# Kernel tuning notes

Measured on AMD Instinct MI355X. Metric: run time of the kernel, lower is better.

## Reference

```python
import jax, jax.numpy as jnp
import numpy as np

N_NODES = 110
C = 4096  # in_channels = hidden = out_channels


def setup_inputs() -> dict:
    key = jax.random.key(0)
    ks = jax.random.split(key, 8)
    x = jax.random.normal(ks[0], (N_NODES, C), dtype=jnp.float32)
    adj = jax.random.randint(ks[1], (N_NODES, N_NODES), 0, 2, dtype=jnp.int32)
    # torch.nn.Linear weights stored [out_features, in_features]
    W2 = jax.random.normal(ks[2], (C, C), dtype=jnp.float32) / np.sqrt(C)
    b2 = jax.random.normal(ks[3], (C,), dtype=jnp.float32) * 0.01
    W1 = jax.random.normal(ks[4], (2 * C, C), dtype=jnp.float32) / np.sqrt(2 * C)
    b1 = jax.random.normal(ks[5], (C,), dtype=jnp.float32) * 0.01
    Wl = jax.random.normal(ks[6], (N_NODES, N_NODES), dtype=jnp.float32) / np.sqrt(N_NODES)
    bl = jax.random.normal(ks[7], (N_NODES,), dtype=jnp.float32) * 0.01
    # note: W1 is stored [in=2C, out=C]; W2 [in=C, out=C]; Wl [in=110, out=110]
    return {"x": x, "adj": adj, "W2": W2, "b2": b2, "W1": W1, "b1": b1, "Wl": Wl, "bl": bl}


def reference(x, adj, W2, b2, W1, b1, Wl, bl):
    # FeatGraphConv: h = lin2(x)
    h = x @ W2 + b2  # [N, C]
    # edge_index.nonzero(): adjacency -> edge list (i=src, j=dst); mean-aggregate
    # h[src] at dst. Dense equivalent: column-normalized mask matmul.
    mask = (adj != 0).astype(x.dtype)  # [N, N]
    deg = mask.sum(axis=0)  # in-degree of each target node j
    aggr = (mask.T @ h) / jnp.maximum(deg, 1.0)[:, None]  # [N, C]; 0 for isolated nodes (PyG mean)
    # update: lin1(cat(h, aggr)) then relu (in RegGNN.forward)
    out = jax.nn.relu(jnp.concatenate([h, aggr], axis=1) @ W1 + b1)  # [N, C]
    # x.t(); lin(110,110); x.t()
    out = (out.T @ Wl.T + bl).T  # [N, C]
    return out
```

## Files before the change

### kernel.cpp

```cpp
#include <hip/hip_runtime.h>
#include <hip/hip_fp16.h>

#define C 4096
#define NN 110
#define MPAD 112
#define BN 128
#define BK 64
#define KCHUNK 512
#define NIT (KCHUNK / BK)
#define LDSTR 72
#define BSTR 64

typedef _Float16 f16x8 __attribute__((ext_vector_type(8)));
typedef float fx4 __attribute__((ext_vector_type(4)));

__global__ __launch_bounds__(256)
void prep1_kernel(const float* __restrict__ x, _Float16* __restrict__ A1) {
    int idx = blockIdx.x * 256 + threadIdx.x;
    int n = idx >> 11;
    union { _Float16 h[2]; unsigned u; } pk;
    pk.u = 0;
    if (n < NN) {
        float2 v = *(const float2*)(x + 2 * (size_t)idx);
        pk.h[0] = (_Float16)v.x;
        pk.h[1] = (_Float16)v.y;
    }
    ((unsigned*)A1)[idx] = pk.u;
}

__global__ __launch_bounds__(256, 2)
void mm_kernel(const _Float16* __restrict__ A, const float* __restrict__ B,
               float* __restrict__ Cacc, int lda) {
    __shared__ _Float16 As[2][MPAD * LDSTR];
    __shared__ _Float16 Bs[2][BN * BSTR];

    const int t    = threadIdx.x;
    const int j0   = blockIdx.x * BN;
    const int k0   = blockIdx.y * KCHUNK;
    const int w    = t >> 6;
    const int L    = t & 63;
    const int l15  = L & 15;
    const int q    = L >> 4;
    const int bc   = t & 127;
    const int bgq  = t >> 7;
    const int bswz = bc & 7;

    int arow[4], ako[4];
    bool aval[4];
#pragma unroll
    for (int i = 0; i < 4; ++i) {
        int idx = t + i * 256;
        aval[i] = (idx < MPAD * (BK / 8));
        int id2 = aval[i] ? idx : 0;
        arow[i] = id2 >> 3;
        ako[i]  = (id2 & 7) << 3;
    }

    fx4 acc[7][2];
#pragma unroll
    for (int mt = 0; mt < 7; ++mt)
#pragma unroll
        for (int nt = 0; nt < 2; ++nt)
            acc[mt][nt] = (fx4){0.f, 0.f, 0.f, 0.f};

    f16x8 av[4];
    float bv[32];

#define STAGE(kc_)                                                             \
    {                                                                          \
        _Pragma("unroll")                                                      \
        for (int i = 0; i < 4; ++i)                                            \
            av[i] = *(const f16x8*)(A + (size_t)arow[i] * lda + (k0 + (kc_)) + ako[i]); \
        _Pragma("unroll")                                                      \
        for (int p = 0; p < 16; ++p) {                                         \
            int r = (bgq * 16 + p) * 2;                                        \
            bv[2 * p]     = B[(size_t)(k0 + (kc_) + r) * C + j0 + bc];         \
            bv[2 * p + 1] = B[(size_t)(k0 + (kc_) + r + 1) * C + j0 + bc];     \
        }                                                                      \
    }

#define COMMIT(b_)                                                             \
    {                                                                          \
        _Pragma("unroll")                                                      \
        for (int i = 0; i < 4; ++i)                                            \
            if (aval[i])                                                       \
                *(f16x8*)(As[b_] + arow[i] * LDSTR + ako[i]) = av[i];          \
        _Pragma("unroll")                                                      \
        for (int p = 0; p < 16; ++p) {                                         \
            int P = bgq * 16 + p;                                              \
            union { _Float16 h[2]; unsigned u; } pk;                           \
            pk.h[0] = (_Float16)bv[2 * p];                                     \
            pk.h[1] = (_Float16)bv[2 * p + 1];                                 \
            *(unsigned*)(Bs[b_] + bc * BSTR + (((P >> 2) ^ bswz) << 3)         \
                         + ((P & 3) << 1)) = pk.u;                             \
        }                                                                      \
    }

    STAGE(0);
    COMMIT(0);
    __syncthreads();

    for (int it = 0; it < NIT; ++it) {
        if (it + 1 < NIT) STAGE((it + 1) * BK);
        const int b = it & 1;
#pragma unroll
        for (int s = 0; s < 2; ++s) {
            const int ko = s * 32 + q * 8;
            f16x8 bfrag[2];
#pragma unroll
            for (int nt = 0; nt < 2; ++nt) {
                const int cW = w * 32 + nt * 16 + l15;
                bfrag[nt] = *(const f16x8*)(Bs[b] + cW * BSTR
                                + ((((s << 2) + q) ^ (l15 & 7)) << 3));
            }
#pragma unroll
            for (int mt = 0; mt < 7; ++mt) {
                f16x8 afrag = *(const f16x8*)(As[b] + (mt * 16 + l15) * LDSTR + ko);
#pragma unroll
                for (int nt = 0; nt < 2; ++nt)
                    acc[mt][nt] = __builtin_amdgcn_mfma_f32_16x16x32_f16(
                        afrag, bfrag[nt], acc[mt][nt], 0, 0, 0);
            }
        }
        if (it + 1 < NIT) COMMIT((it + 1) & 1);
        __syncthreads();
    }

#pragma unroll
    for (int mt = 0; mt < 7; ++mt)
#pragma unroll
        for (int nt = 0; nt < 2; ++nt) {
            const int col = j0 + w * 32 + nt * 16 + l15;
#pragma unroll
            for (int r = 0; r < 4; ++r) {
                int row = mt * 16 + q * 4 + r;
                if (row < NN)
                    atomicAdd(&Cacc[(size_t)row * C + col], acc[mt][nt][r]);
            }
        }
#undef STAGE
#undef COMMIT
}

__global__ __launch_bounds__(256)
void agg_kernel(const float* __restrict__ h_raw, const int* __restrict__ adj,
                const float* __restrict__ b2, _Float16* __restrict__ A3) {
    __shared__ float hb[NN * 16];
    __shared__ unsigned long long mlo[NN], mhi[NN];
    __shared__ float degs[NN];
    const int t  = threadIdx.x;
    const int c0 = blockIdx.x * 16;

    for (int idx = t; idx < NN * 8; idx += 256) {
        int n = idx >> 3, cp = (idx & 7) << 1;
        float2 v = *(const float2*)(h_raw + (size_t)n * C + c0 + cp);
        float v0 = v.x + b2[c0 + cp];
        float v1 = v.y + b2[c0 + cp + 1];
        hb[n * 16 + cp]     = v0;
        hb[n * 16 + cp + 1] = v1;
        union { _Float16 h[2]; unsigned u; } pk;
        pk.h[0] = (_Float16)v0;
        pk.h[1] = (_Float16)v1;
        *(unsigned*)(A3 + (size_t)n * (2 * C) + c0 + cp) = pk.u;
    }
    if (t < 32) {
        int n  = NN + (t >> 4);
        int hs = (t >> 3) & 1;
        int cp = (t & 7) << 1;
        *(unsigned*)(A3 + (size_t)n * (2 * C) + hs * C + c0 + cp) = 0u;
    }
    if (t < NN) {
        int j = t;
        unsigned long long lo = 0, hi = 0;
        int dg = 0;
        for (int i = 0; i < 64; ++i) {
            int m = (adj[i * NN + j] != 0);
            lo |= ((unsigned long long)m) << i; dg += m;
        }
        for (int i = 64; i < NN; ++i) {
            int m = (adj[i * NN + j] != 0);
            hi |= ((unsigned long long)m) << (i - 64); dg += m;
        }
        mlo[j] = lo; mhi[j] = hi;
        degs[j] = (float)(dg > 0 ? dg : 1);
    }
    __syncthreads();
    for (int idx = t; idx < NN * 8; idx += 256) {
        int j = idx >> 3, cp = (idx & 7) << 1;
        unsigned long long lo = mlo[j], hi = mhi[j];
        float a0 = 0.f, a1 = 0.f;
        for (int i = 0; i < 64; ++i)
            if ((lo >> i) & 1) { a0 += hb[i * 16 + cp]; a1 += hb[i * 16 + cp + 1]; }
        for (int i = 64; i < NN; ++i)
            if ((hi >> (i - 64)) & 1) { a0 += hb[i * 16 + cp]; a1 += hb[i * 16 + cp + 1]; }
        union { _Float16 h[2]; unsigned u; } pk;
        pk.h[0] = (_Float16)(a0 / degs[j]);
        pk.h[1] = (_Float16)(a1 / degs[j]);
        *(unsigned*)(A3 + (size_t)j * (2 * C) + C + c0 + cp) = pk.u;
    }
}

__global__ __launch_bounds__(256)
void fin_kernel(const float* __restrict__ z_raw, const float* __restrict__ b1,
                const float* __restrict__ Wl, const float* __restrict__ bl,
                float* __restrict__ out) {
    __shared__ float zs[NN * 64];
    const int t  = threadIdx.x;
    const int c0 = blockIdx.x * 64;
    const int c  = t & 63;

    for (int idx = t; idx < NN * 64; idx += 256) {
        int k = idx >> 6, cc = idx & 63;
        float v = z_raw[(size_t)k * C + c0 + cc] + b1[c0 + cc];
        zs[idx] = fmaxf(v, 0.f);
    }
    __syncthreads();
    for (int jj = 0; jj < 7; ++jj) {
        int j = blockIdx.y * 28 + jj * 4 + (t >> 6);
        if (j < NN) {
            float a = bl[j];
#pragma unroll 2
            for (int k = 0; k < NN; ++k)
                a += Wl[j * NN + k] * zs[k * 64 + c];
            out[(size_t)j * C + c0 + c] = a;
        }
    }
}

extern "C" void kernel_launch(void* const* d_in, const int* in_sizes, int n_in,
                              void* d_out, int out_size, void* d_ws, size_t ws_size,
                              hipStream_t stream) {
    const float* x   = (const float*)d_in[0];
    const int*   adj = (const int*)d_in[1];
    const float* W2  = (const float*)d_in[2];
    const float* b2  = (const float*)d_in[3];
    const float* W1  = (const float*)d_in[4];
    const float* b1  = (const float*)d_in[5];
    const float* Wl  = (const float*)d_in[6];
    const float* bl  = (const float*)d_in[7];
    float* out = (float*)d_out;

    char* ws = (char*)d_ws;
    float*    h_raw = (float*)(ws);
    float*    z_raw = (float*)(ws + 1802240);
    _Float16* A1    = (_Float16*)(ws + 3604480);
    _Float16* A3    = (_Float16*)(ws + 4521984);

    hipMemsetAsync(d_ws, 0, 3604480, stream);
    prep1_kernel<<<(MPAD * C / 2) / 256, 256, 0, stream>>>(x, A1);
    mm_kernel<<<dim3(C / BN, C / KCHUNK), 256, 0, stream>>>(A1, W2, h_raw, C);
    agg_kernel<<<C / 16, 256, 0, stream>>>(h_raw, adj, b2, A3);
    mm_kernel<<<dim3(C / BN, (2 * C) / KCHUNK), 256, 0, stream>>>(A3, W1, z_raw, 2 * C);
    fin_kernel<<<dim3(C / 64, 4), 256, 0, stream>>>(z_raw, b1, Wl, bl, out);
}
```

Before: 358.7 us.

## Retile GEMM to 64-column blocks with A read directly from global memory

New measurement: 387.2 us. +8.0%, slower.

```diff
diff --git a/kernel.cpp b/kernel.cpp
--- a/kernel.cpp
+++ b/kernel.cpp
@@ -4,15 +4,10 @@
 #define C 4096
 #define NN 110
 #define MPAD 112
-#define BN 128
-#define BK 64
-#define KCHUNK 512
-#define NIT (KCHUNK / BK)
-#define LDSTR 72
-#define BSTR 64
 
 typedef _Float16 f16x8 __attribute__((ext_vector_type(8)));
 typedef float fx4 __attribute__((ext_vector_type(4)));
+typedef unsigned long long ull;
 
 __global__ __launch_bounds__(256)
 void prep1_kernel(const float* __restrict__ x, _Float16* __restrict__ A1) {
@@ -28,126 +23,120 @@
     ((unsigned*)A1)[idx] = pk.u;
 }
 
-__global__ __launch_bounds__(256, 2)
+__global__ __launch_bounds__(128)
+void maskprep_kernel(const int* __restrict__ adj, ull* __restrict__ mlo,
+                     ull* __restrict__ mhi, float* __restrict__ degs) {
+    int j = threadIdx.x;
+    if (j < NN) {
+        ull lo = 0, hi = 0; int dg = 0;
+        for (int i = 0; i < 64; ++i) {
+            int m = (adj[i * NN + j] != 0);
+            lo |= ((ull)m) << i; dg += m;
+        }
+        for (int i = 64; i < NN; ++i) {
+            int m = (adj[i * NN + j] != 0);
+            hi |= ((ull)m) << (i - 64); dg += m;
+        }
+        mlo[j] = lo; mhi[j] = hi;
+        degs[j] = (float)(dg > 0 ? dg : 1);
+    }
+}
+
+template<int NITER>
+__global__ __launch_bounds__(256, 3)
 void mm_kernel(const _Float16* __restrict__ A, const float* __restrict__ B,
                float* __restrict__ Cacc, int lda) {
-    __shared__ _Float16 As[2][MPAD * LDSTR];
-    __shared__ _Float16 Bs[2][BN * BSTR];
-
-    const int t    = threadIdx.x;
-    const int j0   = blockIdx.x * BN;
-    const int k0   = blockIdx.y * KCHUNK;
-    const int w    = t >> 6;
-    const int L    = t & 63;
-    const int l15  = L & 15;
-    const int q    = L >> 4;
-    const int bc   = t & 127;
-    const int bgq  = t >> 7;
-    const int bswz = bc & 7;
-
-    int arow[4], ako[4];
-    bool aval[4];
-#pragma unroll
-    for (int i = 0; i < 4; ++i) {
-        int idx = t + i * 256;
-        aval[i] = (idx < MPAD * (BK / 8));
-        int id2 = aval[i] ? idx : 0;
-        arow[i] = id2 >> 3;
-        ako[i]  = (id2 & 7) << 3;
-    }
-
-    fx4 acc[7][2];
+    __shared__ __align__(16) _Float16 Bs[2][64 * 64];
+
+    const int t   = threadIdx.x;
+    const int j0  = blockIdx.x * 64;
+    const int k0  = blockIdx.y * (NITER * 64);
+    const int w   = t >> 6;
+    const int L   = t & 63;
+    const int l15 = L & 15;
+    const int q   = L >> 4;
+    const int sc  = t & 63;
+    const int kg  = t >> 6;
+    const int swz = sc & 7;
+
+    fx4 acc[7];
+#pragma unroll
+    for (int mt = 0; mt < 7; ++mt) acc[mt] = (fx4){0.f, 0.f, 0.f, 0.f};
+
+    const float*    Bp  = B + (size_t)k0 * C + j0 + sc;
+    const _Float16* Ap  = A + (size_t)l15 * lda + k0;
+    _Float16*       BsW = &Bs[0][0] + sc * 64;
+    const _Float16* BsR = &Bs[0][0] + (w * 16 + l15) * 64;
+
+    float bva[16], bvb[16];
+
+#define LOADB(dst, ch)                                                         \
+    { _Pragma("unroll")                                                        \
+      for (int p = 0; p < 16; ++p)                                             \
+          dst[p] = Bp[(size_t)((ch) * 64 + kg * 16 + p) * C]; }
+
+#define COMMITB(src, buf)                                                      \
+    { _Pragma("unroll")                                                        \
+      for (int p2 = 0; p2 < 2; ++p2) {                                         \
+          f16x8 hv;                                                            \
+          _Pragma("unroll")                                                    \
+          for (int e = 0; e < 8; ++e) hv[e] = (_Float16)src[p2 * 8 + e];       \
+          *(f16x8*)(BsW + (buf) * 4096 + (((kg * 2 + p2) ^ swz) << 3)) = hv;   \
+      } }
+
+    LOADB(bva, 0);
+    COMMITB(bva, 0);
+    LOADB(bva, 1);
+    __syncthreads();
+
+#pragma unroll
+    for (int it = 0; it < NITER; ++it) {
+        f16x8 af[2][7];
+#pragma unroll
+        for (int s = 0; s < 2; ++s)
+#pragma unroll
+            for (int mt = 0; mt < 7; ++mt)
+                af[s][mt] = *(const f16x8*)(Ap + (size_t)mt * 16 * lda
+                                            + it * 64 + s * 32 + q * 8);
+        __builtin_amdgcn_sched_barrier(0);
+        if (it + 2 < NITER) {
+            if (it & 1) { LOADB(bva, it + 2); } else { LOADB(bvb, it + 2); }
+        }
+        __builtin_amdgcn_sched_barrier(0);
+#pragma unroll
+        for (int s = 0; s < 2; ++s) {
+            f16x8 bf = *(const f16x8*)(BsR + (it & 1) * 4096
+                            + ((((s << 2) + q) ^ (l15 & 7)) << 3));
+#pragma unroll
+            for (int mt = 0; mt < 7; ++mt)
+                acc[mt] = __builtin_amdgcn_mfma_f32_16x16x32_f16(
+                    af[s][mt], bf, acc[mt], 0, 0, 0);
+        }
+        if (it + 1 < NITER) {
+            if (it & 1) { COMMITB(bvb, (it + 1) & 1); }
+            else        { COMMITB(bva, (it + 1) & 1); }
+        }
+        __syncthreads();
+    }
+
+    const int col = j0 + w * 16 + l15;
 #pragma unroll
     for (int mt = 0; mt < 7; ++mt)
 #pragma unroll
-        for (int nt = 0; nt < 2; ++nt)
-            acc[mt][nt] = (fx4){0.f, 0.f, 0.f, 0.f};
-
-    f16x8 av[4];
-    float bv[32];
-
-#define STAGE(kc_)                                                             \
-    {                                                                          \
-        _Pragma("unroll")                                                      \
-        for (int i = 0; i < 4; ++i)                                            \
-            av[i] = *(const f16x8*)(A + (size_t)arow[i] * lda + (k0 + (kc_)) + ako[i]); \
-        _Pragma("unroll")                                                      \
-        for (int p = 0; p < 16; ++p) {                                         \
-            int r = (bgq * 16 + p) * 2;                                        \
-            bv[2 * p]     = B[(size_t)(k0 + (kc_) + r) * C + j0 + bc];         \
-            bv[2 * p + 1] = B[(size_t)(k0 + (kc_) + r + 1) * C + j0 + bc];     \
-        }                                                                      \
-    }
-
-#define COMMIT(b_)                                                             \
-    {                                                                          \
-        _Pragma("unroll")                                                      \
-        for (int i = 0; i < 4; ++i)                                            \
-            if (aval[i])                                                       \
-                *(f16x8*)(As[b_] + arow[i] * LDSTR + ako[i]) = av[i];          \
-        _Pragma("unroll")                                                      \
-        for (int p = 0; p < 16; ++p) {                                         \
-            int P = bgq * 16 + p;                                              \
-            union { _Float16 h[2]; unsigned u; } pk;                           \
-            pk.h[0] = (_Float16)bv[2 * p];                                     \
-            pk.h[1] = (_Float16)bv[2 * p + 1];                                 \
-            *(unsigned*)(Bs[b_] + bc * BSTR + (((P >> 2) ^ bswz) << 3)         \
-                         + ((P & 3) << 1)) = pk.u;                             \
-        }                                                                      \
-    }
-
-    STAGE(0);
-    COMMIT(0);
-    __syncthreads();
-
-    for (int it = 0; it < NIT; ++it) {
-        if (it + 1 < NIT) STAGE((it + 1) * BK);
-        const int b = it & 1;
-#pragma unroll
-        for (int s = 0; s < 2; ++s) {
-            const int ko = s * 32 + q * 8;
-            f16x8 bfrag[2];
-#pragma unroll
-            for (int nt = 0; nt < 2; ++nt) {
-                const int cW = w * 32 + nt * 16 + l15;
-                bfrag[nt] = *(const f16x8*)(Bs[b] + cW * BSTR
-                                + ((((s << 2) + q) ^ (l15 & 7)) << 3));
-            }
-#pragma unroll
-            for (int mt = 0; mt < 7; ++mt) {
-                f16x8 afrag = *(const f16x8*)(As[b] + (mt * 16 + l15) * LDSTR + ko);
-#pragma unroll
-                for (int nt = 0; nt < 2; ++nt)
-                    acc[mt][nt] = __builtin_amdgcn_mfma_f32_16x16x32_f16(
-                        afrag, bfrag[nt], acc[mt][nt], 0, 0, 0);
-            }
-        }
-        if (it + 1 < NIT) COMMIT((it + 1) & 1);
-        __syncthreads();
-    }
-
-#pragma unroll
-    for (int mt = 0; mt < 7; ++mt)
-#pragma unroll
-        for (int nt = 0; nt < 2; ++nt) {
-            const int col = j0 + w * 32 + nt * 16 + l15;
-#pragma unroll
-            for (int r = 0; r < 4; ++r) {
-                int row = mt * 16 + q * 4 + r;
-                if (row < NN)
-                    atomicAdd(&Cacc[(size_t)row * C + col], acc[mt][nt][r]);
-            }
-        }
-#undef STAGE
-#undef COMMIT
+        for (int r = 0; r < 4; ++r) {
+            int row = mt * 16 + q * 4 + r;
+            if (row < NN)
+                atomicAdd(&Cacc[(size_t)row * C + col], acc[mt][r]);
+        }
+#undef LOADB
+#undef COMMITB
 }
 
 __global__ __launch_bounds__(256)
-void agg_kernel(const float* __restrict__ h_raw, const int* __restrict__ adj,
+void agg_kernel(const float* __restrict__ h_raw, const ull* __restrict__ gmlo,
+                const ull* __restrict__ gmhi, const float* __restrict__ gdegs,
                 const float* __restrict__ b2, _Float16* __restrict__ A3) {
     __shared__ float hb[NN * 16];
-    __shared__ unsigned long long mlo[NN], mhi[NN];
-    __shared__ float degs[NN];
     const int t  = threadIdx.x;
     const int c0 = blockIdx.x * 16;
 
@@ -169,33 +158,19 @@
         int cp = (t & 7) << 1;
         *(unsigned*)(A3 + (size_t)n * (2 * C) + hs * C + c0 + cp) = 0u;
     }
-    if (t < NN) {
-        int j = t;
-        unsigned long long lo = 0, hi = 0;
-        int dg = 0;
-        for (int i = 0; i < 64; ++i) {
-            int m = (adj[i * NN + j] != 0);
-            lo |= ((unsigned long long)m) << i; dg += m;
-        }
-        for (int i = 64; i < NN; ++i) {
-            int m = (adj[i * NN + j] != 0);
-            hi |= ((unsigned long long)m) << (i - 64); dg += m;
-        }
-        mlo[j] = lo; mhi[j] = hi;
-        degs[j] = (float)(dg > 0 ? dg : 1);
-    }
     __syncthreads();
     for (int idx = t; idx < NN * 8; idx += 256) {
         int j = idx >> 3, cp = (idx & 7) << 1;
-        unsigned long long lo = mlo[j], hi = mhi[j];
+        ull lo = gmlo[j], hi = gmhi[j];
+        float dg = gdegs[j];
         float a0 = 0.f, a1 = 0.f;
         for (int i = 0; i < 64; ++i)
             if ((lo >> i) & 1) { a0 += hb[i * 16 + cp]; a1 += hb[i * 16 + cp + 1]; }
         for (int i = 64; i < NN; ++i)
             if ((hi >> (i - 64)) & 1) { a0 += hb[i * 16 + cp]; a1 += hb[i * 16 + cp + 1]; }
         union { _Float16 h[2]; unsigned u; } pk;
-        pk.h[0] = (_Float16)(a0 / degs[j]);
-        pk.h[1] = (_Float16)(a1 / degs[j]);
+        pk.h[0] = (_Float16)(a0 / dg);
+        pk.h[1] = (_Float16)(a1 / dg);
         *(unsigned*)(A3 + (size_t)j * (2 * C) + C + c0 + cp) = pk.u;
     }
 }
@@ -245,11 +220,15 @@
     float*    z_raw = (float*)(ws + 1802240);
     _Float16* A1    = (_Float16*)(ws + 3604480);
     _Float16* A3    = (_Float16*)(ws + 4521984);
+    ull*      mlo   = (ull*)(ws + 6356992);
+    ull*      mhi   = (ull*)(ws + 6357872);
+    float*    degs  = (float*)(ws + 6358752);
 
     hipMemsetAsync(d_ws, 0, 3604480, stream);
     prep1_kernel<<<(MPAD * C / 2) / 256, 256, 0, stream>>>(x, A1);
-    mm_kernel<<<dim3(C / BN, C / KCHUNK), 256, 0, stream>>>(A1, W2, h_raw, C);
-    agg_kernel<<<C / 16, 256, 0, stream>>>(h_raw, adj, b2, A3);
-    mm_kernel<<<dim3(C / BN, (2 * C) / KCHUNK), 256, 0, stream>>>(A3, W1, z_raw, 2 * C);
+    maskprep_kernel<<<1, 128, 0, stream>>>(adj, mlo, mhi, degs);
+    mm_kernel<4><<<dim3(64, 16), 256, 0, stream>>>(A1, W2, h_raw, C);
+    agg_kernel<<<C / 16, 256, 0, stream>>>(h_raw, mlo, mhi, degs, b2, A3);
+    mm_kernel<8><<<dim3(64, 16), 256, 0, stream>>>(A3, W1, z_raw, 2 * C);
     fin_kernel<<<dim3(C / 64, 4), 256, 0, stream>>>(z_raw, b1, Wl, bl, out);
 }
```
